# Optimization experiments

Hardware: AMD Instinct MI355X
Metric: run time of the kernel (lower is better)

Reference implementation:

```python
import jax, jax.numpy as jnp
import numpy as np

EMBED = 768
NHEADS = 12
HEAD_DIM = EMBED // NHEADS
LA_HEADS = 16
MLP_HID = EMBED * 4
EPS = 1e-5


def setup_inputs() -> dict:
    key = jax.random.key(0)
    ks = jax.random.split(key, 16)
    s = lambda fan_in: 1.0 / np.sqrt(fan_in)
    inp = {
        "x": jax.random.normal(ks[0], (64, 197, EMBED), dtype=jnp.float32),
        "norm1_g": jnp.ones((EMBED,), jnp.float32),
        "norm1_b": jnp.zeros((EMBED,), jnp.float32),
        "qkv_w": jax.random.normal(ks[1], (3 * EMBED, EMBED), jnp.float32) * s(EMBED),
        "qkv_b": jnp.zeros((3 * EMBED,), jnp.float32),
        "proj_w": jax.random.normal(ks[2], (EMBED, EMBED), jnp.float32) * s(EMBED),
        "proj_b": jnp.zeros((EMBED,), jnp.float32),
        "norm2_g": jnp.ones((EMBED,), jnp.float32),
        "norm2_b": jnp.zeros((EMBED,), jnp.float32),
        "fc1_w": jax.random.normal(ks[3], (MLP_HID, EMBED), jnp.float32) * s(EMBED),
        "fc1_b": jnp.zeros((MLP_HID,), jnp.float32),
        "fc2_w": jax.random.normal(ks[4], (EMBED, MLP_HID), jnp.float32) * s(MLP_HID),
        "fc2_b": jnp.zeros((EMBED,), jnp.float32),
        # LA params: f1 Conv2d(16,1,1) -> weight [16]; f2 Conv2d(1,16,1) -> weight [16]; v Conv2d(2,1,1) -> weight [2]
        "f1_w": jax.random.normal(ks[5], (LA_HEADS,), jnp.float32) * s(LA_HEADS),
        "f1_b": jnp.zeros((1,), jnp.float32),
        "f2_w": jax.random.normal(ks[6], (LA_HEADS,), jnp.float32),
        "f2_b": jnp.zeros((LA_HEADS,), jnp.float32),
        "v_w": jax.random.normal(ks[7], (2,), jnp.float32) * s(2),
        "v_b": jnp.zeros((1,), jnp.float32),
    }
    return inp


def _layernorm(x, g, b):
    mu = x.mean(-1, keepdims=True)
    var = jnp.mean((x - mu) ** 2, -1, keepdims=True)
    return (x - mu) * jax.lax.rsqrt(var + EPS) * g + b


def _la(x, f1_w, f1_b, f2_w, f2_b, v_w, v_b):
    # x: [B, C=768, 14, 14]; 16 channel groups of 48, pooled over 7x7 grid of 2x2 patches
    B, C, H, W = x.shape
    g = C // LA_HEADS
    xr = x.reshape(B, LA_HEADS, g, 7, 2, 7, 2)
    means = xr.mean(axis=(2, 4, 6))            # [B,16,7,7]
    maxs = xr.max(axis=(2, 4, 6))              # [B,16,7,7]

    def channel_mlp(t):  # f2(relu(f1(t))), 1x1 convs across the 16 "head" channels
        h = jnp.einsum('bchw,c->bhw', t, f1_w) + f1_b[0]
        h = jax.nn.relu(h)
        return h[:, None, :, :] * f2_w[None, :, None, None] + f2_b[None, :, None, None]

    m = channel_mlp(means)
    mx = channel_mlp(maxs)
    fusion = v_w[0] * m + v_w[1] * mx + v_b[0]   # [B,16,7,7]
    # bilinear upsample 7x7 -> 14x14, align_corners=False (half-pixel centers)
    fusion = jax.image.resize(fusion, (B, LA_HEADS, 14, 14), method='bilinear')
    gate = jax.nn.sigmoid(fusion)                # [B,16,14,14]
    out = x.reshape(B, LA_HEADS, g, H, W) * gate[:, :, None, :, :]
    return out.reshape(B, C, H, W) + x


def _attn(x, qkv_w, qkv_b, proj_w, proj_b):
    B, N, D = x.shape
    qkv = x @ qkv_w.T + qkv_b
    qkv = qkv.reshape(B, N, 3, NHEADS, HEAD_DIM).transpose(2, 0, 3, 1, 4)
    q, k, v = qkv[0], qkv[1], qkv[2]             # [B,H,N,hd]
    scores = jnp.einsum('bhnd,bhmd->bhnm', q, k) * (HEAD_DIM ** -0.5)
    a = jax.nn.softmax(scores, axis=-1)
    o = jnp.einsum('bhnm,bhmd->bhnd', a, v)
    o = o.transpose(0, 2, 1, 3).reshape(B, N, D)
    return o @ proj_w.T + proj_b


def reference(x, norm1_g, norm1_b, qkv_w, qkv_b, proj_w, proj_b,
              norm2_g, norm2_b, fc1_w, fc1_b, fc2_w, fc2_b,
              f1_w, f1_b, f2_w, f2_b, v_w, v_b):
    B, N, C = x.shape
    cls_tok = x[:, :1, :]                        # [B,1,C]
    spatial = x[:, 1:, :]                        # [B,196,C]
    H = W = 14
    x_la = spatial.reshape(B, H, W, C).transpose(0, 3, 1, 2)   # [B,C,14,14]
    x_la = _la(x_la, f1_w, f1_b, f2_w, f2_b, v_w, v_b)
    x_la = x_la.reshape(B, C, H * W).transpose(0, 2, 1)        # [B,196,C]
    x_cat = jnp.concatenate([cls_tok, x_la], axis=1)           # [B,197,C]
    x = x + _attn(_layernorm(x_cat, norm1_g, norm1_b), qkv_w, qkv_b, proj_w, proj_b)
    h = _layernorm(x, norm2_g, norm2_b)
    h = jax.nn.gelu(h @ fc1_w.T + fc1_b, approximate=False)
    x = x + (h @ fc2_w.T + fc2_b)
    return x
```

## Files before the change

kernel.cpp:

```cpp
#include <hip/hip_runtime.h>
#include <hip/hip_bf16.h>
#include <math.h>

using bf16 = __hip_bfloat16;
using short8 = __attribute__((ext_vector_type(8))) short;
using floatx4 = __attribute__((ext_vector_type(4))) float;

constexpr int B = 64;
constexpr int N = 197;
constexpr int C = 768;
constexpr int NH = 12;
constexpr int HD = 64;
constexpr int HID = 3072;
constexpr int M = B * N;
constexpr int MPAD = 12672;
constexpr int MT = MPAD / 128;
constexpr int MTP = 104;
constexpr float EPS = 1e-5f;

__device__ __forceinline__ float b2f(bf16 v) { return __bfloat162float(v); }
__device__ __forceinline__ bf16 f2b(float v) { return __float2bfloat16(v); }

typedef const __attribute__((address_space(1))) unsigned int* gas1_t;
typedef __attribute__((address_space(3))) unsigned int* las3_t;
__device__ __forceinline__ void load_lds16(const bf16* g, bf16* l) {
  __builtin_amdgcn_global_load_lds((gas1_t)g, (las3_t)l, 16, 0, 0);
}

__global__ void cvt_wf_kernel(const float* __restrict__ src, bf16* __restrict__ dst,
                              int Nc, int K) {
  int i = blockIdx.x * 256 + threadIdx.x;
  int total = Nc * (K >> 3);
  if (i >= total) return;
  int k8 = i % (K >> 3);
  int n  = i / (K >> 3);
  int kc = k8 >> 2, quad = k8 & 3;
  int nb = n >> 7, nn = n & 127, tp = nn >> 4, l = nn & 15;
  int KC = K >> 5;
  size_t di = (((size_t)nb * KC + kc) * 8 + tp) * 512 + quad * 128 + l * 8;
  const float* s = src + (size_t)n * K + k8 * 8;
  #pragma unroll
  for (int e = 0; e < 8; ++e) dst[di + e] = f2b(s[e]);
}

__device__ __forceinline__ float block_sum(float v, float* red) {
  #pragma unroll
  for (int off = 32; off >= 1; off >>= 1) v += __shfl_xor(v, off, 64);
  int w = threadIdx.x >> 6;
  if ((threadIdx.x & 63) == 0) red[w] = v;
  __syncthreads();
  float r = red[0] + red[1] + red[2] + red[3];
  __syncthreads();
  return r;
}

__global__ void la_pool_kernel(const float* __restrict__ x,
                               const float* __restrict__ f1w, const float* __restrict__ f1bias,
                               const float* __restrict__ f2w, const float* __restrict__ f2bias,
                               const float* __restrict__ vw,  const float* __restrict__ vbias,
                               float* __restrict__ fusion7) {
  int blk = blockIdx.x;
  int b = blk / 49, p = blk % 49;
  int h7 = p / 7, w7 = p % 7;
  int tid = threadIdx.x;
  int head = tid >> 4;
  int j = tid & 15;

  float sum = 0.f, mx = -3.0e38f;
  #pragma unroll
  for (int a = 0; a < 2; ++a) {
    #pragma unroll
    for (int bb = 0; bb < 2; ++bb) {
      int tok = 1 + (2 * h7 + a) * 14 + (2 * w7 + bb);
      const float* row = x + ((size_t)b * N + tok) * C + head * 48;
      #pragma unroll
      for (int s = 0; s < 3; ++s) {
        float v = row[j + 16 * s];
        sum += v;
        mx = fmaxf(mx, v);
      }
    }
  }
  #pragma unroll
  for (int off = 8; off >= 1; off >>= 1) {
    sum += __shfl_xor(sum, off, 64);
    mx = fmaxf(mx, __shfl_xor(mx, off, 64));
  }
  __shared__ float s_mean[16], s_max[16];
  if (j == 0) { s_mean[head] = sum / 192.f; s_max[head] = mx; }
  __syncthreads();
  if (tid < 16) {
    float hm = f1bias[0], hx = hm;
    #pragma unroll
    for (int h = 0; h < 16; ++h) {
      float w = f1w[h];
      hm += s_mean[h] * w;
      hx += s_max[h] * w;
    }
    hm = fmaxf(hm, 0.f);
    hx = fmaxf(hx, 0.f);
    float w2 = f2w[tid], b2v = f2bias[tid];
    float m   = hm * w2 + b2v;
    float mxv = hx * w2 + b2v;
    float fus = vw[0] * m + vw[1] * mxv + vbias[0];
    fusion7[((size_t)b * 16 + tid) * 49 + p] = fus;
  }
}

__global__ void gate_ln1_kernel(const float* __restrict__ x, const float* __restrict__ fusion7,
                                const float* __restrict__ g, const float* __restrict__ beta,
                                bf16* __restrict__ ln1) {
  int blk = blockIdx.x;
  int b = blk / N, n = blk % N;
  int tid = threadIdx.x;
  __shared__ float gates[16];
  __shared__ float red[4];

  if (tid < 16) {
    if (n > 0) {
      int hh = (n - 1) / 14, ww = (n - 1) % 14;
      float ch = fminf(fmaxf(hh * 0.5f - 0.25f, 0.f), 6.f);
      float cw = fminf(fmaxf(ww * 0.5f - 0.25f, 0.f), 6.f);
      int h0 = (int)floorf(ch); int h1 = min(h0 + 1, 6); float fh = ch - (float)h0;
      int w0 = (int)floorf(cw); int w1 = min(w0 + 1, 6); float fw = cw - (float)w0;
      const float* fp = fusion7 + ((size_t)b * 16 + tid) * 49;
      float v00 = fp[h0 * 7 + w0], v01 = fp[h0 * 7 + w1];
      float v10 = fp[h1 * 7 + w0], v11 = fp[h1 * 7 + w1];
      float v = (1.f - fh) * ((1.f - fw) * v00 + fw * v01)
              + fh        * ((1.f - fw) * v10 + fw * v11);
      gates[tid] = 1.f / (1.f + expf(-v));
    } else {
      gates[tid] = 0.f;
    }
  }
  __syncthreads();

  const float* xr = x + ((size_t)b * N + n) * C;
  float v[3];
  #pragma unroll
  for (int s = 0; s < 3; ++s) {
    int c = tid + 256 * s;
    v[s] = xr[c] * (1.f + gates[c / 48]);
  }
  float mu = block_sum(v[0] + v[1] + v[2], red) * (1.f / 768.f);
  float d0 = v[0] - mu, d1 = v[1] - mu, d2 = v[2] - mu;
  float var = block_sum(d0 * d0 + d1 * d1 + d2 * d2, red) * (1.f / 768.f);
  float rs = rsqrtf(var + EPS);
  bf16* orow = ln1 + ((size_t)b * N + n) * C;
  #pragma unroll
  for (int s = 0; s < 3; ++s) {
    int c = tid + 256 * s;
    orow[c] = f2b((v[s] - mu) * rs * g[c] + beta[c]);
  }
}

__global__ void ln_bf16_kernel(const bf16* __restrict__ xin,
                               const float* __restrict__ g, const float* __restrict__ beta,
                               bf16* __restrict__ out) {
  int row = blockIdx.x;
  int tid = threadIdx.x;
  __shared__ float red[4];
  const bf16* xr = xin + (size_t)row * C;
  float v[3];
  #pragma unroll
  for (int s = 0; s < 3; ++s) v[s] = b2f(xr[tid + 256 * s]);
  float mu = block_sum(v[0] + v[1] + v[2], red) * (1.f / 768.f);
  float d0 = v[0] - mu, d1 = v[1] - mu, d2 = v[2] - mu;
  float var = block_sum(d0 * d0 + d1 * d1 + d2 * d2, red) * (1.f / 768.f);
  float rs = rsqrtf(var + EPS);
  bf16* orow = out + (size_t)row * C;
  #pragma unroll
  for (int s = 0; s < 3; ++s) {
    int c = tid + 256 * s;
    orow[c] = f2b((v[s] - mu) * rs * g[c] + beta[c]);
  }
}

template <int EPI, int K>
__global__ void __launch_bounds__(256, 3)
gemm128(const bf16* __restrict__ A, const bf16* __restrict__ Wf,
        const float* __restrict__ bias,
        const float* __restrict__ resF, const bf16* __restrict__ resB,
        bf16* __restrict__ outB, float* __restrict__ outF, int Nc) {
  constexpr int KC = K >> 5;
  static_assert(KC % 6 == 0, "KC must be divisible by 6 for the unroll");
  constexpr int CW = (K == 768) ? 6 : 3;
  constexpr int PERCH = 13 * CW;
  int nx = Nc >> 7;
  int g = blockIdx.x;
  int c = g & 7;
  int t = g >> 3;
  int ch = t / PERCH;
  int r  = t % PERCH;
  int j  = r / CW;
  int x  = ch * CW + (r % CW);
  int y  = c + 8 * j;
  if (y >= MT) return;
  int m0 = y * 128;
  int n0 = x * 128;

  __shared__ __align__(16) char smem[24576];
  bf16* sA = (bf16*)smem;

  int tid = threadIdx.x;
  int wave = tid >> 6, lane = tid & 63, quad = lane >> 4, l16 = lane & 15;

  int ln16 = lane >> 2, seg = lane & 3;
  int sw = seg ^ ((ln16 >> 1) & 3);
  const bf16* gA = A + (size_t)(m0 + wave * 32 + ln16) * K + sw * 8;

  int wm = (wave & 1) * 64, wn = (wave >> 1) * 64;
  int csw = (l16 >> 1) & 3;
  int tp0 = wn >> 4;

  const bf16* gBf = Wf + ((size_t)(n0 >> 7) * KC) * 4096 + (size_t)tp0 * 512 + lane * 8;

  floatx4 acc[4][4] = {};

  bf16* dA0 = sA + (wave * 32) * 32;

  auto stageA = [&](const bf16* gAp, int bufOff) {
    load_lds16(gAp, dA0 + bufOff);
    load_lds16(gAp + (size_t)16 * K, dA0 + bufOff + 16 * 32);
  };

  short8 bA0, bA1, bA2, bA3, bB0, bB1, bB2, bB3;
  stageA(gA, 0);
  bA0 = *reinterpret_cast<const short8*>(gBf);
  bA1 = *reinterpret_cast<const short8*>(gBf + 512);
  bA2 = *reinterpret_cast<const short8*>(gBf + 1024);
  bA3 = *reinterpret_cast<const short8*>(gBf + 1536);
  stageA(gA + 32, 4096);

  const bf16* gAs = gA + 64;
  const bf16* gBs = gBf + 4096;

  const bf16* aRd = sA + (wm + l16) * 32 + (quad ^ csw) * 8;

#define GEMM_BODY(bufOff, stageBufOff, R0, R1, R2, R3, L0, L1, L2, L3, DOSTAGE, DOLOADB, LAST) \
  do {                                                                          \
    if (LAST) { asm volatile("s_waitcnt vmcnt(4) lgkmcnt(0)" ::: "memory"); }   \
    else      { asm volatile("s_waitcnt vmcnt(6) lgkmcnt(0)" ::: "memory"); }   \
    __builtin_amdgcn_s_barrier();                                               \
    __builtin_amdgcn_sched_barrier(0);                                          \
    short8 af0 = *reinterpret_cast<const short8*>(aRd + (bufOff));              \
    short8 af1 = *reinterpret_cast<const short8*>(aRd + (bufOff) + 512);        \
    short8 af2 = *reinterpret_cast<const short8*>(aRd + (bufOff) + 1024);       \
    short8 af3 = *reinterpret_cast<const short8*>(aRd + (bufOff) + 1536);       \
    if (DOLOADB) {                                                              \
      L0 = *reinterpret_cast<const short8*>(gBs);                               \
      L1 = *reinterpret_cast<const short8*>(gBs + 512);                         \
      L2 = *reinterpret_cast<const short8*>(gBs + 1024);                        \
      L3 = *reinterpret_cast<const short8*>(gBs + 1536);                        \
      gBs += 4096;                                                              \
    }                                                                           \
    if (DOSTAGE) { stageA(gAs, (stageBufOff)); gAs += 32; }                     \
    __builtin_amdgcn_s_setprio(1);                                              \
    acc[0][0] = __builtin_amdgcn_mfma_f32_16x16x32_bf16(af0, R0, acc[0][0], 0, 0, 0); \
    acc[0][1] = __builtin_amdgcn_mfma_f32_16x16x32_bf16(af0, R1, acc[0][1], 0, 0, 0); \
    acc[0][2] = __builtin_amdgcn_mfma_f32_16x16x32_bf16(af0, R2, acc[0][2], 0, 0, 0); \
    acc[0][3] = __builtin_amdgcn_mfma_f32_16x16x32_bf16(af0, R3, acc[0][3], 0, 0, 0); \
    acc[1][0] = __builtin_amdgcn_mfma_f32_16x16x32_bf16(af1, R0, acc[1][0], 0, 0, 0); \
    acc[1][1] = __builtin_amdgcn_mfma_f32_16x16x32_bf16(af1, R1, acc[1][1], 0, 0, 0); \
    acc[1][2] = __builtin_amdgcn_mfma_f32_16x16x32_bf16(af1, R2, acc[1][2], 0, 0, 0); \
    acc[1][3] = __builtin_amdgcn_mfma_f32_16x16x32_bf16(af1, R3, acc[1][3], 0, 0, 0); \
    acc[2][0] = __builtin_amdgcn_mfma_f32_16x16x32_bf16(af2, R0, acc[2][0], 0, 0, 0); \
    acc[2][1] = __builtin_amdgcn_mfma_f32_16x16x32_bf16(af2, R1, acc[2][1], 0, 0, 0); \
    acc[2][2] = __builtin_amdgcn_mfma_f32_16x16x32_bf16(af2, R2, acc[2][2], 0, 0, 0); \
    acc[2][3] = __builtin_amdgcn_mfma_f32_16x16x32_bf16(af2, R3, acc[2][3], 0, 0, 0); \
    acc[3][0] = __builtin_amdgcn_mfma_f32_16x16x32_bf16(af3, R0, acc[3][0], 0, 0, 0); \
    acc[3][1] = __builtin_amdgcn_mfma_f32_16x16x32_bf16(af3, R1, acc[3][1], 0, 0, 0); \
    acc[3][2] = __builtin_amdgcn_mfma_f32_16x16x32_bf16(af3, R2, acc[3][2], 0, 0, 0); \
    acc[3][3] = __builtin_amdgcn_mfma_f32_16x16x32_bf16(af3, R3, acc[3][3], 0, 0, 0); \
    __builtin_amdgcn_s_setprio(0);                                              \
  } while (0)

  for (int kc0 = 0; kc0 < KC; kc0 += 6) {
    bool last = (kc0 + 6 >= KC);
    GEMM_BODY(0,    8192, bA0, bA1, bA2, bA3, bB0, bB1, bB2, bB3, true,  true,  false);
    GEMM_BODY(4096, 0,    bB0, bB1, bB2, bB3, bA0, bA1, bA2, bA3, true,  true,  false);
    GEMM_BODY(8192, 4096, bA0, bA1, bA2, bA3, bB0, bB1, bB2, bB3, true,  true,  false);
    GEMM_BODY(0,    8192, bB0, bB1, bB2, bB3, bA0, bA1, bA2, bA3, true,  true,  false);
    GEMM_BODY(4096, 0,    bA0, bA1, bA2, bA3, bB0, bB1, bB2, bB3, !last, true,  false);
    GEMM_BODY(8192, 4096, bB0, bB1, bB2, bB3, bA0, bA1, bA2, bA3, !last, !last, last);
  }
#undef GEMM_BODY

  if (!resF && !resB && outB) {
    bf16* sC = (bf16*)smem;
    constexpr int SCS = 136;
    #pragma unroll
    for (int half = 0; half < 2; ++half) {
      __syncthreads();
      if (wm == half * 64) {
        #pragma unroll
        for (int t2 = 0; t2 < 4; ++t2) {
          int col = wn + t2 * 16 + l16;
          float bv = bias[n0 + col];
          #pragma unroll
          for (int s = 0; s < 4; ++s) {
            int rowb = s * 16 + quad * 4;
            #pragma unroll
            for (int r2 = 0; r2 < 4; ++r2) {
              float v = acc[s][t2][r2] + bv;
              if (EPI == 1) v = 0.5f * v * (1.f + erff(v * 0.7071067811865475f));
              sC[(rowb + r2) * SCS + col] = f2b(v);
            }
          }
        }
      }
      __syncthreads();
      int rl = tid >> 4, cl = tid & 15;
      #pragma unroll
      for (int i = 0; i < 4; ++i) {
        int row = i * 16 + rl;
        int gr = m0 + half * 64 + row;
        if (gr < M) {
          short8 vv = *reinterpret_cast<const short8*>(sC + row * SCS + cl * 8);
          *reinterpret_cast<short8*>(outB + (size_t)gr * Nc + n0 + cl * 8) = vv;
        }
      }
    }
  } else {
    #pragma unroll
    for (int t2 = 0; t2 < 4; ++t2) {
      int col = n0 + wn + t2 * 16 + l16;
      float bv = bias[col];
      #pragma unroll
      for (int s = 0; s < 4; ++s) {
        int rowb = m0 + wm + s * 16 + quad * 4;
        #pragma unroll
        for (int r2 = 0; r2 < 4; ++r2) {
          int row = rowb + r2;
          if (row < M) {
            float v = acc[s][t2][r2] + bv;
            if (EPI == 1) v = 0.5f * v * (1.f + erff(v * 0.7071067811865475f));
            size_t idx = (size_t)row * Nc + col;
            if (resF) v += resF[idx];
            if (resB) v += b2f(resB[idx]);
            if (outF) outF[idx] = v;
            if (outB) outB[idx] = f2b(v);
          }
        }
      }
    }
  }
}

__global__ void __launch_bounds__(256, 2)
attn_mfma_kernel(const bf16* __restrict__ qkv, bf16* __restrict__ attn_o) {
  int bh = blockIdx.x;
  int h = bh % NH, b = bh / NH;
  int tid = threadIdx.x;
  int wave = tid >> 6, lane = tid & 63, quad = lane >> 4, l16 = lane & 15;

  __shared__ __align__(16) bf16 sVt[64][232];
  __shared__ __align__(16) bf16 sP[4][16][232];

  const bf16* base = qkv + (size_t)b * N * 2304 + h * 64;

  {
    int d = tid & 63;
    for (int m = tid >> 6; m < 224; m += 4) {
      sVt[d][m] = (m < N) ? base[(size_t)m * 2304 + 1536 + d] : f2b(0.f);
    }
  }
  __syncthreads();

  const float scale = 0.125f;

  for (int qt = wave; qt < 13; qt += 4) {
    int qr = min(qt * 16 + l16, N - 1);
    const bf16* qp = base + (size_t)qr * 2304;
    short8 aq0 = *reinterpret_cast<const short8*>(qp + quad * 8);
    short8 aq1 = *reinterpret_cast<const short8*>(qp + 32 + quad * 8);

    floatx4 s[13];
    short8 bk0c, bk1c;
    {
      int kr = min(l16, N - 1);
      const bf16* kp = base + (size_t)kr * 2304 + 768;
      bk0c = *reinterpret_cast<const short8*>(kp + quad * 8);
      bk1c = *reinterpret_cast<const short8*>(kp + 32 + quad * 8);
    }
    #pragma unroll
    for (int kt = 0; kt < 13; ++kt) {
      short8 bk0n, bk1n;
      if (kt < 12) {
        int kr = min((kt + 1) * 16 + l16, N - 1);
        const bf16* kp = base + (size_t)kr * 2304 + 768;
        bk0n = *reinterpret_cast<const short8*>(kp + quad * 8);
        bk1n = *reinterpret_cast<const short8*>(kp + 32 + quad * 8);
      }
      floatx4 acc = floatx4{0.f, 0.f, 0.f, 0.f};
      acc = __builtin_amdgcn_mfma_f32_16x16x32_bf16(aq0, bk0c, acc, 0, 0, 0);
      acc = __builtin_amdgcn_mfma_f32_16x16x32_bf16(aq1, bk1c, acc, 0, 0, 0);
      s[kt] = acc;
      if (kt < 12) { bk0c = bk0n; bk1c = bk1n; }
    }

    bool cv[13];
    #pragma unroll
    for (int kt = 0; kt < 13; ++kt) cv[kt] = (kt * 16 + l16) < N;

    float mx[4] = {-3.0e38f, -3.0e38f, -3.0e38f, -3.0e38f};
    #pragma unroll
    for (int kt = 0; kt < 13; ++kt) {
      #pragma unroll
      for (int r = 0; r < 4; ++r) {
        float sv = s[kt][r] * scale;
        s[kt][r] = sv;
        if (cv[kt]) mx[r] = fmaxf(mx[r], sv);
      }
    }
    #pragma unroll
    for (int off = 8; off >= 1; off >>= 1) {
      #pragma unroll
      for (int r = 0; r < 4; ++r) mx[r] = fmaxf(mx[r], __shfl_xor(mx[r], off, 64));
    }
    float sum[4] = {0.f, 0.f, 0.f, 0.f};
    #pragma unroll
    for (int kt = 0; kt < 13; ++kt) {
      #pragma unroll
      for (int r = 0; r < 4; ++r) {
        float e = cv[kt] ? __expf(s[kt][r] - mx[r]) : 0.f;
        s[kt][r] = e;
        sum[r] += e;
      }
    }
    #pragma unroll
    for (int off = 8; off >= 1; off >>= 1) {
      #pragma unroll
      for (int r = 0; r < 4; ++r) sum[r] += __shfl_xor(sum[r], off, 64);
    }
    float inv[4];
    #pragma unroll
    for (int r = 0; r < 4; ++r) inv[r] = 1.f / sum[r];

    #pragma unroll
    for (int kt = 0; kt < 13; ++kt) {
      #pragma unroll
      for (int r = 0; r < 4; ++r)
        sP[wave][quad * 4 + r][kt * 16 + l16] = f2b(s[kt][r]);
    }
    #pragma unroll
    for (int r = 0; r < 4; ++r)
      sP[wave][quad * 4 + r][208 + l16] = f2b(0.f);

    floatx4 o[4] = {floatx4{0,0,0,0}, floatx4{0,0,0,0}, floatx4{0,0,0,0}, floatx4{0,0,0,0}};
    #pragma unroll
    for (int c = 0; c < 7; ++c) {
      short8 ap = *reinterpret_cast<const short8*>(&sP[wave][l16][c * 32 + quad * 8]);
      #pragma unroll
      for (int t = 0; t < 4; ++t) {
        short8 bv = *reinterpret_cast<const short8*>(&sVt[t * 16 + l16][c * 32 + quad * 8]);
        o[t] = __builtin_amdgcn_mfma_f32_16x16x32_bf16(ap, bv, o[t], 0, 0, 0);
      }
    }

    asm volatile("s_waitcnt lgkmcnt(0)" ::: "memory");
    bf16* sO = &sP[wave][0][0];
    constexpr int SOS = 72;
    #pragma unroll
    for (int t = 0; t < 4; ++t) {
      #pragma unroll
      for (int r = 0; r < 4; ++r)
        sO[(quad * 4 + r) * SOS + t * 16 + l16] = f2b(o[t][r] * inv[r]);
    }
    asm volatile("s_waitcnt lgkmcnt(0)" ::: "memory");
    int orow = lane >> 3, ocol = (lane & 7) * 8;
    #pragma unroll
    for (int i = 0; i < 2; ++i) {
      int row = i * 8 + orow;
      int qrow = qt * 16 + row;
      if (qrow < N) {
        short8 vv = *reinterpret_cast<const short8*>(sO + row * SOS + ocol);
        *reinterpret_cast<short8*>(attn_o + ((size_t)b * N + qrow) * C + h * 64 + ocol) = vv;
      }
    }
    asm volatile("s_waitcnt lgkmcnt(0)" ::: "memory");
  }
}

extern "C" void kernel_launch(void* const* d_in, const int* in_sizes, int n_in,
                              void* d_out, int out_size, void* d_ws, size_t ws_size,
                              hipStream_t stream) {
  (void)in_sizes; (void)n_in; (void)out_size; (void)ws_size;
  const float* x       = (const float*)d_in[0];
  const float* norm1_g = (const float*)d_in[1];
  const float* norm1_b = (const float*)d_in[2];
  const float* qkv_w   = (const float*)d_in[3];
  const float* qkv_b   = (const float*)d_in[4];
  const float* proj_w  = (const float*)d_in[5];
  const float* proj_b  = (const float*)d_in[6];
  const float* norm2_g = (const float*)d_in[7];
  const float* norm2_b = (const float*)d_in[8];
  const float* fc1_w   = (const float*)d_in[9];
  const float* fc1_b   = (const float*)d_in[10];
  const float* fc2_w   = (const float*)d_in[11];
  const float* fc2_b   = (const float*)d_in[12];
  const float* f1_w    = (const float*)d_in[13];
  const float* f1_b    = (const float*)d_in[14];
  const float* f2_w    = (const float*)d_in[15];
  const float* f2_b    = (const float*)d_in[16];
  const float* v_w     = (const float*)d_in[17];
  const float* v_b     = (const float*)d_in[18];
  float* out = (float*)d_out;

  char* ws = (char*)d_ws;
  float* fusion7 = (float*)(ws + 0);
  bf16*  qkv_wf  = (bf16*)(ws + 262144);
  bf16*  proj_wf = (bf16*)(ws + 3801088);
  bf16*  fc1_wf  = (bf16*)(ws + 4980736);
  bf16*  fc2_wf  = (bf16*)(ws + 9699328);
  bf16*  ln1     = (bf16*)(ws + 14417920);
  bf16*  attn_o  = ln1;
  bf16*  ln2     = ln1;
  bf16*  qkvb    = (bf16*)(ws + 33882112);
  bf16*  hbuf    = qkvb;
  bf16*  x2b     = (bf16*)(ws + 111738880);

  cvt_wf_kernel<<<(2304 * 96 + 255) / 256, 256, 0, stream>>>(qkv_w, qkv_wf, 2304, 768);
  cvt_wf_kernel<<<(768 * 96 + 255) / 256, 256, 0, stream>>>(proj_w, proj_wf, 768, 768);
  cvt_wf_kernel<<<(3072 * 96 + 255) / 256, 256, 0, stream>>>(fc1_w, fc1_wf, 3072, 768);
  cvt_wf_kernel<<<(768 * 384 + 255) / 256, 256, 0, stream>>>(fc2_w, fc2_wf, 768, 3072);

  la_pool_kernel<<<B * 49, 256, 0, stream>>>(x, f1_w, f1_b, f2_w, f2_b, v_w, v_b, fusion7);
  gate_ln1_kernel<<<B * N, 256, 0, stream>>>(x, fusion7, norm1_g, norm1_b, ln1);
  gemm128<0, 768><<<(2304 / 128) * MTP, 256, 0, stream>>>(
      ln1, qkv_wf, qkv_b, nullptr, nullptr, qkvb, nullptr, 2304);
  attn_mfma_kernel<<<B * NH, 256, 0, stream>>>(qkvb, attn_o);
  gemm128<0, 768><<<(768 / 128) * MTP, 256, 0, stream>>>(
      attn_o, proj_wf, proj_b, x, nullptr, x2b, nullptr, 768);
  ln_bf16_kernel<<<M, 256, 0, stream>>>(x2b, norm2_g, norm2_b, ln2);
  gemm128<1, 768><<<(HID / 128) * MTP, 256, 0, stream>>>(
      ln2, fc1_wf, fc1_b, nullptr, nullptr, hbuf, nullptr, HID);
  gemm128<0, 3072><<<(768 / 128) * MTP, 256, 0, stream>>>(
      hbuf, fc2_wf, fc2_b, nullptr, x2b, nullptr, out, 768);
}
```

Before: 610.0 us.

## Enlarge GEMM tiles to 256x128 with 8 waves and LDS-staged weights

Replaces the 128x128, 4-wave GEMM with a 256x128 tile run by 512 threads (8 waves). Weight tiles are now loaded into LDS through global_load_lds and shared by the waves, instead of each wave loading its B fragments directly into registers. The larger tile halves how often the weight tiles are re-fetched per row and doubles per-block work, and out-of-range A rows are clamped to avoid reading past M. In exchange it uses 64KB of LDS per block, which may lower occupancy, and the grid tail shrinks to 50 row tiles.

```diff
diff --git a/kernel.cpp b/kernel.cpp
--- a/kernel.cpp
+++ b/kernel.cpp
@@ -14,8 +14,8 @@
 constexpr int HID = 3072;
 constexpr int M = B * N;
 constexpr int MPAD = 12672;
-constexpr int MT = MPAD / 128;
-constexpr int MTP = 104;
+constexpr int MT256 = 50;
+constexpr int MTP256 = 56;
 constexpr float EPS = 1e-5f;
 
 __device__ __forceinline__ float b2f(bf16 v) { return __bfloat162float(v); }
@@ -177,16 +177,15 @@
 }
 
 template <int EPI, int K>
-__global__ void __launch_bounds__(256, 3)
-gemm128(const bf16* __restrict__ A, const bf16* __restrict__ Wf,
+__global__ void __launch_bounds__(512, 4)
+gemm256(const bf16* __restrict__ A, const bf16* __restrict__ Wf,
         const float* __restrict__ bias,
         const float* __restrict__ resF, const bf16* __restrict__ resB,
         bf16* __restrict__ outB, float* __restrict__ outF, int Nc) {
   constexpr int KC = K >> 5;
   static_assert(KC % 6 == 0, "KC must be divisible by 6 for the unroll");
   constexpr int CW = (K == 768) ? 6 : 3;
-  constexpr int PERCH = 13 * CW;
-  int nx = Nc >> 7;
+  constexpr int PERCH = 7 * CW;
   int g = blockIdx.x;
   int c = g & 7;
   int t = g >> 3;
@@ -195,116 +194,117 @@
   int j  = r / CW;
   int x  = ch * CW + (r % CW);
   int y  = c + 8 * j;
-  if (y >= MT) return;
-  int m0 = y * 128;
+  if (y >= MT256) return;
+  int m0 = y * 256;
   int n0 = x * 128;
 
-  __shared__ __align__(16) char smem[24576];
+  __shared__ __align__(16) char smem[65536];
   bf16* sA = (bf16*)smem;
+  bf16* sB = (bf16*)(smem + 49152);
 
   int tid = threadIdx.x;
   int wave = tid >> 6, lane = tid & 63, quad = lane >> 4, l16 = lane & 15;
 
   int ln16 = lane >> 2, seg = lane & 3;
   int sw = seg ^ ((ln16 >> 1) & 3);
-  const bf16* gA = A + (size_t)(m0 + wave * 32 + ln16) * K + sw * 8;
-
-  int wm = (wave & 1) * 64, wn = (wave >> 1) * 64;
+  int r1 = min(m0 + wave * 32 + ln16, M - 1);
+  int r2c = min(m0 + wave * 32 + 16 + ln16, M - 1);
+  const bf16* gA1s = A + (size_t)r1 * K + sw * 8;
+  const bf16* gA2s = A + (size_t)r2c * K + sw * 8;
+
+  int wm = (wave & 3) * 64, wn = (wave >> 2) * 64;
   int csw = (l16 >> 1) & 3;
-  int tp0 = wn >> 4;
-
-  const bf16* gBf = Wf + ((size_t)(n0 >> 7) * KC) * 4096 + (size_t)tp0 * 512 + lane * 8;
+  int tp0 = (wave >> 2) * 4;
+
+  const bf16* gB0 = Wf + ((size_t)(n0 >> 7) * KC) * 4096 + (size_t)wave * 512 + lane * 8;
 
   floatx4 acc[4][4] = {};
 
-  bf16* dA0 = sA + (wave * 32) * 32;
-
-  auto stageA = [&](const bf16* gAp, int bufOff) {
-    load_lds16(gAp, dA0 + bufOff);
-    load_lds16(gAp + (size_t)16 * K, dA0 + bufOff + 16 * 32);
-  };
-
-  short8 bA0, bA1, bA2, bA3, bB0, bB1, bB2, bB3;
-  stageA(gA, 0);
-  bA0 = *reinterpret_cast<const short8*>(gBf);
-  bA1 = *reinterpret_cast<const short8*>(gBf + 512);
-  bA2 = *reinterpret_cast<const short8*>(gBf + 1024);
-  bA3 = *reinterpret_cast<const short8*>(gBf + 1536);
-  stageA(gA + 32, 4096);
-
-  const bf16* gAs = gA + 64;
-  const bf16* gBs = gBf + 4096;
+  bf16* dA = sA + wave * 1024;
+  bf16* dB = sB + wave * 512;
+
+  load_lds16(gA1s, dA);
+  load_lds16(gA2s, dA + 512);
+  load_lds16(gB0, dB);
+  load_lds16(gA1s + 32, dA + 8192);
+  load_lds16(gA2s + 32, dA + 8192 + 512);
+  gA1s += 64; gA2s += 64;
+  const bf16* gBs = gB0 + 4096;
 
   const bf16* aRd = sA + (wm + l16) * 32 + (quad ^ csw) * 8;
-
-#define GEMM_BODY(bufOff, stageBufOff, R0, R1, R2, R3, L0, L1, L2, L3, DOSTAGE, DOLOADB, LAST) \
+  const bf16* bRd = sB + tp0 * 512 + lane * 8;
+
+#define GEMM_BODY(aOff, bOff, aStOff, bStOff, DOSTA, DOLDB, LAST)               \
   do {                                                                          \
-    if (LAST) { asm volatile("s_waitcnt vmcnt(4) lgkmcnt(0)" ::: "memory"); }   \
-    else      { asm volatile("s_waitcnt vmcnt(6) lgkmcnt(0)" ::: "memory"); }   \
+    if (LAST) { asm volatile("s_waitcnt vmcnt(0) lgkmcnt(0)" ::: "memory"); }   \
+    else      { asm volatile("s_waitcnt vmcnt(2) lgkmcnt(0)" ::: "memory"); }   \
     __builtin_amdgcn_s_barrier();                                               \
     __builtin_amdgcn_sched_barrier(0);                                          \
-    short8 af0 = *reinterpret_cast<const short8*>(aRd + (bufOff));              \
-    short8 af1 = *reinterpret_cast<const short8*>(aRd + (bufOff) + 512);        \
-    short8 af2 = *reinterpret_cast<const short8*>(aRd + (bufOff) + 1024);       \
-    short8 af3 = *reinterpret_cast<const short8*>(aRd + (bufOff) + 1536);       \
-    if (DOLOADB) {                                                              \
-      L0 = *reinterpret_cast<const short8*>(gBs);                               \
-      L1 = *reinterpret_cast<const short8*>(gBs + 512);                         \
-      L2 = *reinterpret_cast<const short8*>(gBs + 1024);                        \
-      L3 = *reinterpret_cast<const short8*>(gBs + 1536);                        \
-      gBs += 4096;                                                              \
+    short8 af0 = *reinterpret_cast<const short8*>(aRd + (aOff));                \
+    short8 af1 = *reinterpret_cast<const short8*>(aRd + (aOff) + 512);          \
+    short8 af2 = *reinterpret_cast<const short8*>(aRd + (aOff) + 1024);         \
+    short8 af3 = *reinterpret_cast<const short8*>(aRd + (aOff) + 1536);         \
+    short8 bw0 = *reinterpret_cast<const short8*>(bRd + (bOff));                \
+    short8 bw1 = *reinterpret_cast<const short8*>(bRd + (bOff) + 512);          \
+    short8 bw2 = *reinterpret_cast<const short8*>(bRd + (bOff) + 1024);         \
+    short8 bw3 = *reinterpret_cast<const short8*>(bRd + (bOff) + 1536);         \
+    if (DOLDB) { load_lds16(gBs, dB + (bStOff)); gBs += 4096; }                 \
+    if (DOSTA) {                                                                \
+      load_lds16(gA1s, dA + (aStOff));                                          \
+      load_lds16(gA2s, dA + (aStOff) + 512);                                    \
+      gA1s += 32; gA2s += 32;                                                   \
     }                                                                           \
-    if (DOSTAGE) { stageA(gAs, (stageBufOff)); gAs += 32; }                     \
     __builtin_amdgcn_s_setprio(1);                                              \
-    acc[0][0] = __builtin_amdgcn_mfma_f32_16x16x32_bf16(af0, R0, acc[0][0], 0, 0, 0); \
-    acc[0][1] = __builtin_amdgcn_mfma_f32_16x16x32_bf16(af0, R1, acc[0][1], 0, 0, 0); \
-    acc[0][2] = __builtin_amdgcn_mfma_f32_16x16x32_bf16(af0, R2, acc[0][2], 0, 0, 0); \
-    acc[0][3] = __builtin_amdgcn_mfma_f32_16x16x32_bf16(af0, R3, acc[0][3], 0, 0, 0); \
-    acc[1][0] = __builtin_amdgcn_mfma_f32_16x16x32_bf16(af1, R0, acc[1][0], 0, 0, 0); \
-    acc[1][1] = __builtin_amdgcn_mfma_f32_16x16x32_bf16(af1, R1, acc[1][1], 0, 0, 0); \
-    acc[1][2] = __builtin_amdgcn_mfma_f32_16x16x32_bf16(af1, R2, acc[1][2], 0, 0, 0); \
-    acc[1][3] = __builtin_amdgcn_mfma_f32_16x16x32_bf16(af1, R3, acc[1][3], 0, 0, 0); \
-    acc[2][0] = __builtin_amdgcn_mfma_f32_16x16x32_bf16(af2, R0, acc[2][0], 0, 0, 0); \
-    acc[2][1] = __builtin_amdgcn_mfma_f32_16x16x32_bf16(af2, R1, acc[2][1], 0, 0, 0); \
-    acc[2][2] = __builtin_amdgcn_mfma_f32_16x16x32_bf16(af2, R2, acc[2][2], 0, 0, 0); \
-    acc[2][3] = __builtin_amdgcn_mfma_f32_16x16x32_bf16(af2, R3, acc[2][3], 0, 0, 0); \
-    acc[3][0] = __builtin_amdgcn_mfma_f32_16x16x32_bf16(af3, R0, acc[3][0], 0, 0, 0); \
-    acc[3][1] = __builtin_amdgcn_mfma_f32_16x16x32_bf16(af3, R1, acc[3][1], 0, 0, 0); \
-    acc[3][2] = __builtin_amdgcn_mfma_f32_16x16x32_bf16(af3, R2, acc[3][2], 0, 0, 0); \
-    acc[3][3] = __builtin_amdgcn_mfma_f32_16x16x32_bf16(af3, R3, acc[3][3], 0, 0, 0); \
+    acc[0][0] = __builtin_amdgcn_mfma_f32_16x16x32_bf16(af0, bw0, acc[0][0], 0, 0, 0); \
+    acc[0][1] = __builtin_amdgcn_mfma_f32_16x16x32_bf16(af0, bw1, acc[0][1], 0, 0, 0); \
+    acc[0][2] = __builtin_amdgcn_mfma_f32_16x16x32_bf16(af0, bw2, acc[0][2], 0, 0, 0); \
+    acc[0][3] = __builtin_amdgcn_mfma_f32_16x16x32_bf16(af0, bw3, acc[0][3], 0, 0, 0); \
+    acc[1][0] = __builtin_amdgcn_mfma_f32_16x16x32_bf16(af1, bw0, acc[1][0], 0, 0, 0); \
+    acc[1][1] = __builtin_amdgcn_mfma_f32_16x16x32_bf16(af1, bw1, acc[1][1], 0, 0, 0); \
+    acc[1][2] = __builtin_amdgcn_mfma_f32_16x16x32_bf16(af1, bw2, acc[1][2], 0, 0, 0); \
+    acc[1][3] = __builtin_amdgcn_mfma_f32_16x16x32_bf16(af1, bw3, acc[1][3], 0, 0, 0); \
+    acc[2][0] = __builtin_amdgcn_mfma_f32_16x16x32_bf16(af2, bw0, acc[2][0], 0, 0, 0); \
+    acc[2][1] = __builtin_amdgcn_mfma_f32_16x16x32_bf16(af2, bw1, acc[2][1], 0, 0, 0); \
+    acc[2][2] = __builtin_amdgcn_mfma_f32_16x16x32_bf16(af2, bw2, acc[2][2], 0, 0, 0); \
+    acc[2][3] = __builtin_amdgcn_mfma_f32_16x16x32_bf16(af2, bw3, acc[2][3], 0, 0, 0); \
+    acc[3][0] = __builtin_amdgcn_mfma_f32_16x16x32_bf16(af3, bw0, acc[3][0], 0, 0, 0); \
+    acc[3][1] = __builtin_amdgcn_mfma_f32_16x16x32_bf16(af3, bw1, acc[3][1], 0, 0, 0); \
+    acc[3][2] = __builtin_amdgcn_mfma_f32_16x16x32_bf16(af3, bw2, acc[3][2], 0, 0, 0); \
+    acc[3][3] = __builtin_amdgcn_mfma_f32_16x16x32_bf16(af3, bw3, acc[3][3], 0, 0, 0); \
     __builtin_amdgcn_s_setprio(0);                                              \
   } while (0)
 
   for (int kc0 = 0; kc0 < KC; kc0 += 6) {
-    bool last = (kc0 + 6 >= KC);
-    GEMM_BODY(0,    8192, bA0, bA1, bA2, bA3, bB0, bB1, bB2, bB3, true,  true,  false);
-    GEMM_BODY(4096, 0,    bB0, bB1, bB2, bB3, bA0, bA1, bA2, bA3, true,  true,  false);
-    GEMM_BODY(8192, 4096, bA0, bA1, bA2, bA3, bB0, bB1, bB2, bB3, true,  true,  false);
-    GEMM_BODY(0,    8192, bB0, bB1, bB2, bB3, bA0, bA1, bA2, bA3, true,  true,  false);
-    GEMM_BODY(4096, 0,    bA0, bA1, bA2, bA3, bB0, bB1, bB2, bB3, !last, true,  false);
-    GEMM_BODY(8192, 4096, bB0, bB1, bB2, bB3, bA0, bA1, bA2, bA3, !last, !last, last);
+    bool lg = (kc0 + 6 >= KC);
+    GEMM_BODY(0,     0,    16384, 4096, true, true, false);
+    GEMM_BODY(8192,  4096, 0,     0,    true, true, false);
+    GEMM_BODY(16384, 0,    8192,  4096, true, true, false);
+    GEMM_BODY(0,     4096, 16384, 0,    true, true, false);
+    GEMM_BODY(8192,  0,    0,     4096, !lg,  true, false);
+    GEMM_BODY(16384, 4096, 8192,  0,    !lg,  !lg,  lg);
   }
 #undef GEMM_BODY
 
   if (!resF && !resB && outB) {
     bf16* sC = (bf16*)smem;
     constexpr int SCS = 136;
+    int q = wave & 3;
     #pragma unroll
     for (int half = 0; half < 2; ++half) {
       __syncthreads();
-      if (wm == half * 64) {
+      if ((q >> 1) == half) {
         #pragma unroll
         for (int t2 = 0; t2 < 4; ++t2) {
           int col = wn + t2 * 16 + l16;
           float bv = bias[n0 + col];
           #pragma unroll
           for (int s = 0; s < 4; ++s) {
-            int rowb = s * 16 + quad * 4;
+            int rowb = (q & 1) * 64 + s * 16 + quad * 4;
             #pragma unroll
-            for (int r2 = 0; r2 < 4; ++r2) {
-              float v = acc[s][t2][r2] + bv;
+            for (int r3 = 0; r3 < 4; ++r3) {
+              float v = acc[s][t2][r3] + bv;
               if (EPI == 1) v = 0.5f * v * (1.f + erff(v * 0.7071067811865475f));
-              sC[(rowb + r2) * SCS + col] = f2b(v);
+              sC[(rowb + r3) * SCS + col] = f2b(v);
             }
           }
         }
@@ -313,8 +313,8 @@
       int rl = tid >> 4, cl = tid & 15;
       #pragma unroll
       for (int i = 0; i < 4; ++i) {
-        int row = i * 16 + rl;
-        int gr = m0 + half * 64 + row;
+        int row = i * 32 + rl;
+        int gr = m0 + half * 128 + row;
         if (gr < M) {
           short8 vv = *reinterpret_cast<const short8*>(sC + row * SCS + cl * 8);
           *reinterpret_cast<short8*>(outB + (size_t)gr * Nc + n0 + cl * 8) = vv;
@@ -330,10 +330,10 @@
       for (int s = 0; s < 4; ++s) {
         int rowb = m0 + wm + s * 16 + quad * 4;
         #pragma unroll
-        for (int r2 = 0; r2 < 4; ++r2) {
-          int row = rowb + r2;
+        for (int r3 = 0; r3 < 4; ++r3) {
+          int row = rowb + r3;
           if (row < M) {
-            float v = acc[s][t2][r2] + bv;
+            float v = acc[s][t2][r3] + bv;
             if (EPI == 1) v = 0.5f * v * (1.f + erff(v * 0.7071067811865475f));
             size_t idx = (size_t)row * Nc + col;
             if (resF) v += resF[idx];
@@ -527,14 +527,14 @@
 
   la_pool_kernel<<<B * 49, 256, 0, stream>>>(x, f1_w, f1_b, f2_w, f2_b, v_w, v_b, fusion7);
   gate_ln1_kernel<<<B * N, 256, 0, stream>>>(x, fusion7, norm1_g, norm1_b, ln1);
-  gemm128<0, 768><<<(2304 / 128) * MTP, 256, 0, stream>>>(
+  gemm256<0, 768><<<(2304 / 128) * MTP256, 512, 0, stream>>>(
       ln1, qkv_wf, qkv_b, nullptr, nullptr, qkvb, nullptr, 2304);
   attn_mfma_kernel<<<B * NH, 256, 0, stream>>>(qkvb, attn_o);
-  gemm128<0, 768><<<(768 / 128) * MTP, 256, 0, stream>>>(
+  gemm256<0, 768><<<(768 / 128) * MTP256, 512, 0, stream>>>(
       attn_o, proj_wf, proj_b, x, nullptr, x2b, nullptr, 768);
   ln_bf16_kernel<<<M, 256, 0, stream>>>(x2b, norm2_g, norm2_b, ln2);
-  gemm128<1, 768><<<(HID / 128) * MTP, 256, 0, stream>>>(
+  gemm256<1, 768><<<(HID / 128) * MTP256, 512, 0, stream>>>(
       ln2, fc1_wf, fc1_b, nullptr, nullptr, hbuf, nullptr, HID);
-  gemm128<0, 3072><<<(768 / 128) * MTP, 256, 0, stream>>>(
+  gemm256<0, 3072><<<(768 / 128) * MTP256, 512, 0, stream>>>(
       hbuf, fc2_wf, fc2_b, nullptr, x2b, nullptr, out, 768);
 }
```

New measurement: 587.7 us. 1.04x faster.
